# Optimization experiments

Measured on AMD Instinct MI355X. Metric: run time of the kernel, lower is better.

## Reference

```python
import jax, jax.numpy as jnp
import numpy as np

N, F, H, E = 100000, 128, 128, 3200000
EPS = 1e-5


def setup_inputs() -> dict:
    key = jax.random.key(0)
    ks = jax.random.split(key, 16)
    g = lambda k, shape, fan_in: jax.random.normal(k, shape, jnp.float32) / np.sqrt(fan_in)
    inp = {
        'x': jax.random.normal(ks[0], (N, F), jnp.float32),
        'edge_index': jax.random.randint(ks[1], (2, E), 0, N, jnp.int64),
        # SAGEConv params: lin_l (aggregated-neighbor path, has bias), lin_r (root path, no bias)
        'W1l': g(ks[2], (F, H), F), 'b1': jnp.zeros((H,), jnp.float32), 'W1r': g(ks[3], (F, H), F),
        'W2l': g(ks[4], (H, H), H), 'b2': jnp.zeros((H,), jnp.float32), 'W2r': g(ks[5], (H, H), H),
        'W3l': g(ks[6], (H, H), H), 'b3': jnp.zeros((H,), jnp.float32), 'W3r': g(ks[7], (H, H), H),
        'W4l': g(ks[8], (H, 1), H), 'b4': jnp.zeros((1,), jnp.float32), 'W4r': g(ks[9], (H, 1), H),
        # BatchNorm affine params
        'g1': jnp.ones((H,), jnp.float32), 'be1': jnp.zeros((H,), jnp.float32),
        'g2': jnp.ones((H,), jnp.float32), 'be2': jnp.zeros((H,), jnp.float32),
        'g3': jnp.ones((H,), jnp.float32), 'be3': jnp.zeros((H,), jnp.float32),
        # shared residual linear
        'Wlin': g(ks[10], (H, H), H), 'blin': jnp.zeros((H,), jnp.float32),
    }
    return inp


def _sage(x, src, dst, Wl, b, Wr):
    # mean aggregation of source features at destination nodes
    n = x.shape[0]
    s = jax.ops.segment_sum(x[src], dst, num_segments=n)          # [N, d]
    cnt = jax.ops.segment_sum(jnp.ones_like(dst, x.dtype), dst, num_segments=n)
    agg = s / jnp.maximum(cnt, 1.0)[:, None]
    return agg @ Wl + b + x @ Wr


def _bn(x, gamma, beta):
    # training-mode batch norm over node dim (biased variance, as torch)
    mu = x.mean(0)
    var = jnp.mean((x - mu) ** 2, axis=0)
    return gamma * (x - mu) * jax.lax.rsqrt(var + EPS) + beta


def reference(x, edge_index, W1l, b1, W1r, W2l, b2, W2r, W3l, b3, W3r,
              W4l, b4, W4r, g1, be1, g2, be2, g3, be3, Wlin, blin):
    src, dst = edge_index[0], edge_index[1]
    # dropout is identity (eval-mode reference)
    x1 = jax.nn.elu(_bn(_sage(x, src, dst, W1l, b1, W1r), g1, be1))
    x2 = jax.nn.elu(_bn(_sage(x1, src, dst, W2l, b2, W2r), g2, be2))
    x2 = x2 + x1 @ Wlin + blin
    x3 = jax.nn.elu(_bn(_sage(x2, src, dst, W3l, b3, W3r), g3, be3))
    x3 = x3 + x2 @ Wlin + blin
    x4 = _sage(x3, src, dst, W4l, b4, W4r)  # [N, 1]
    return jnp.squeeze(x4, -1)
```

## Files before the change

kernel.cpp:

```cpp
#include <hip/hip_runtime.h>
#include <hip/hip_bf16.h>
#include <math.h>

#define BN_EPS 1e-5f
#define BSTRIDE 96

typedef __attribute__((ext_vector_type(8))) short bf16x8;
typedef __attribute__((ext_vector_type(4))) float f32x4;
typedef unsigned int uint32;

__device__ __forceinline__ unsigned bf16rne(float f) {
  unsigned u = __float_as_uint(f);
  unsigned r = u + 0x7fffu + ((u >> 16) & 1u);
  return r >> 16;
}
__device__ __forceinline__ float bf2f_lo(uint32 u) { return __uint_as_float(u << 16); }
__device__ __forceinline__ float bf2f_hi(uint32 u) { return __uint_as_float(u & 0xffff0000u); }
__device__ __forceinline__ uint32 packbf2(float a, float b) {
  return bf16rne(a) | (bf16rne(b) << 16);
}

__device__ __forceinline__ int edge_at(const int* __restrict__ ei, long long idx, int is64) {
  return is64 ? ei[2 * idx] : ei[idx];
}

__global__ void init_kernel(const int* __restrict__ ei, long long E, int* __restrict__ flag,
                            int* __restrict__ cnt, float* __restrict__ bnsum, int N) {
  if (blockIdx.x == 0) {
    __shared__ int found;
    int t = threadIdx.x;
    if (t == 0) found = 0;
    __syncthreads();
    long long npairs = E < 1024 ? E : 1024;
    for (long long p = t; p < npairs; p += blockDim.x)
      if (ei[2 * p + 1] != 0) found = 1;
    __syncthreads();
    if (t == 0) *flag = found ? 0 : 1;
    return;
  }
  long long i = (blockIdx.x - 1) * (long long)blockDim.x + threadIdx.x;
  if (i < N) cnt[i] = 0;
  else if (i < (long long)N + 64 * 256) bnsum[i - N] = 0.f;
}

__launch_bounds__(256)
__global__ void build_kernel(const int* __restrict__ ei, long long E,
                             const int* __restrict__ flag,
                             int* __restrict__ cnt, int* __restrict__ bkt,
                             const float* __restrict__ x, uint32* __restrict__ xb,
                             long long nf4,
                             const float* __restrict__ Wa, const float* __restrict__ Wb,
                             const float* __restrict__ Wc, const float* __restrict__ Wd,
                             const float* __restrict__ We, const float* __restrict__ Wf,
                             const float* __restrict__ Wg, ushort* __restrict__ Wp,
                             long long K3) {
  long long b = blockIdx.x;
  if (b >= K3) {
    int rb = (int)(b - K3);
    int wi = rb >> 3;
    const float* W = wi == 0 ? Wa : wi == 1 ? Wb : wi == 2 ? Wc : wi == 3 ? Wd
                   : wi == 4 ? We : wi == 5 ? Wf : Wg;
    ushort* dst = Wp + (size_t)wi * 16384;
    int s = (rb & 7) * 256 + threadIdx.x;
    int nt = s >> 8, rem = s & 255, ks = rem >> 6, lane = rem & 63;
    int q = lane >> 4, l16 = lane & 15;
    int kbase = ks * 32 + q * 8, c = nt * 16 + l16;
    uint32 o[4];
#pragma unroll
    for (int jp = 0; jp < 4; ++jp) {
      float fa = W[(size_t)(kbase + 2 * jp) * 128 + c];
      float fb = W[(size_t)(kbase + 2 * jp + 1) * 128 + c];
      o[jp] = packbf2(fa, fb);
    }
    ((uint4*)dst)[s] = make_uint4(o[0], o[1], o[2], o[3]);
    return;
  }
  int role = (int)(b % 3);
  long long id = b / 3;
  if (role == 0) {
    long long g = id * 256 + threadIdx.x;
    long long e0 = 2 * g;
    if (e0 >= E) return;
    int is64 = *flag;
    bool h1 = (e0 + 1 < E);
    int s0, s1 = 0, d0, d1 = 0;
    if (is64 && !(E & 1)) {
      int4 sv = ((const int4*)ei)[g];
      int4 dv = ((const int4*)(ei + 2 * E))[g];
      s0 = sv.x; s1 = sv.z;
      d0 = dv.x; d1 = dv.z;
    } else {
      s0 = edge_at(ei, e0, is64);
      d0 = edge_at(ei, E + e0, is64);
      if (h1) {
        s1 = edge_at(ei, e0 + 1, is64);
        d1 = edge_at(ei, E + e0 + 1, is64);
      }
    }
    int r0 = atomicAdd(&cnt[d0], 1);
    if (r0 < BSTRIDE) bkt[(size_t)d0 * BSTRIDE + r0] = s0;
    if (h1) {
      int r1 = atomicAdd(&cnt[d1], 1);
      if (r1 < BSTRIDE) bkt[(size_t)d1 * BSTRIDE + r1] = s1;
    }
  } else {
    long long i = (id * 2 + (role - 1)) * 256 + threadIdx.x;
    if (i < nf4) {
      float4 f = ((const float4*)x)[i];
      uint2 o2;
      o2.x = packbf2(f.x, f.y);
      o2.y = packbf2(f.z, f.w);
      ((uint2*)xb)[i] = o2;
    }
  }
}

__global__ void aggregate_bf16_kernel(const uint32* __restrict__ X, const int* __restrict__ cnt,
                                      const int* __restrict__ bkt, uint32* __restrict__ out,
                                      int N) {
  int gw = (int)((blockIdx.x * (long long)blockDim.x + threadIdx.x) >> 6);
  int lane = threadIdx.x & 63;
  if (gw >= N) return;
  int deg = cnt[gw];
  if (deg > BSTRIDE) deg = BSTRIDE;
  int b = gw * BSTRIDE, e = b + deg;
  int sub = lane & 15, grp = lane >> 4;
  const uint4* X4 = (const uint4*)X;
  float acc[8];
#pragma unroll
  for (int j = 0; j < 8; ++j) acc[j] = 0.f;
  for (int i = b; i < e; i += 32) {
    uint4 v[8];
#pragma unroll
    for (int u = 0; u < 8; ++u) {
      int ii = i + u * 4 + grp;
      v[u] = make_uint4(0, 0, 0, 0);
      if (ii < e) { int s = bkt[ii]; v[u] = X4[(size_t)s * 16 + sub]; }
    }
#pragma unroll
    for (int u = 0; u < 8; ++u) {
      acc[0] += bf2f_lo(v[u].x); acc[1] += bf2f_hi(v[u].x);
      acc[2] += bf2f_lo(v[u].y); acc[3] += bf2f_hi(v[u].y);
      acc[4] += bf2f_lo(v[u].z); acc[5] += bf2f_hi(v[u].z);
      acc[6] += bf2f_lo(v[u].w); acc[7] += bf2f_hi(v[u].w);
    }
  }
#pragma unroll
  for (int j = 0; j < 8; ++j) {
    acc[j] += __shfl_xor(acc[j], 16, 64);
    acc[j] += __shfl_xor(acc[j], 32, 64);
  }
  if (grp == 0) {
    float inv = 1.0f / fmaxf((float)deg, 1.0f);
    uint4 o;
    o.x = packbf2(acc[0] * inv, acc[1] * inv);
    o.y = packbf2(acc[2] * inv, acc[3] * inv);
    o.z = packbf2(acc[4] * inv, acc[5] * inv);
    o.w = packbf2(acc[6] * inv, acc[7] * inv);
    ((uint4*)out)[(size_t)gw * 16 + sub] = o;
  }
}

__launch_bounds__(256)
__global__ void gemm_mfma_kernel(const ushort* __restrict__ A1, const ushort* __restrict__ W1p,
                                 const ushort* __restrict__ A2, const ushort* __restrict__ W2p,
                                 const ushort* __restrict__ W3p,
                                 const float* __restrict__ bias, const float* __restrict__ rbias,
                                 ushort* __restrict__ Y, ushort* __restrict__ R,
                                 float* __restrict__ bnsum, int N) {
  __shared__ float sred[16][128];
  int t = threadIdx.x;
  int w = t >> 6, lane = t & 63;
  int quad = lane >> 4, l16 = lane & 15;
  int row0 = blockIdx.x * 64 + w * 16;

  f32x4 accY[8], accR[8];
#pragma unroll
  for (int nt = 0; nt < 8; ++nt) {
    accY[nt][0] = accY[nt][1] = accY[nt][2] = accY[nt][3] = 0.f;
    accR[nt][0] = accR[nt][1] = accR[nt][2] = accR[nt][3] = 0.f;
  }

  int rowA = row0 + l16;
  if (rowA > N - 1) rowA = N - 1;
  const ushort* a1p = A1 + (size_t)rowA * 128 + quad * 8;
  const ushort* a2p = A2 + (size_t)rowA * 128 + quad * 8;
  const int haveR = (W3p != nullptr);

#pragma unroll
  for (int ks = 0; ks < 4; ++ks) {
    bf16x8 a = *(const bf16x8*)(a1p + ks * 32);
#pragma unroll
    for (int nt = 0; nt < 8; ++nt) {
      bf16x8 b = *(const bf16x8*)(W1p + ((size_t)(nt * 4 + ks) * 64 + lane) * 8);
      accY[nt] = __builtin_amdgcn_mfma_f32_16x16x32_bf16(a, b, accY[nt], 0, 0, 0);
    }
  }
#pragma unroll
  for (int ks = 0; ks < 4; ++ks) {
    bf16x8 a = *(const bf16x8*)(a2p + ks * 32);
#pragma unroll
    for (int nt = 0; nt < 8; ++nt) {
      bf16x8 b = *(const bf16x8*)(W2p + ((size_t)(nt * 4 + ks) * 64 + lane) * 8);
      accY[nt] = __builtin_amdgcn_mfma_f32_16x16x32_bf16(a, b, accY[nt], 0, 0, 0);
    }
    if (haveR) {
#pragma unroll
      for (int nt = 0; nt < 8; ++nt) {
        bf16x8 b = *(const bf16x8*)(W3p + ((size_t)(nt * 4 + ks) * 64 + lane) * 8);
        accR[nt] = __builtin_amdgcn_mfma_f32_16x16x32_bf16(a, b, accR[nt], 0, 0, 0);
      }
    }
  }

  float s1v[8], s2v[8];
#pragma unroll
  for (int nt = 0; nt < 8; ++nt) {
    int c = nt * 16 + l16;
    float bv = bias[c];
    s1v[nt] = 0.f; s2v[nt] = 0.f;
#pragma unroll
    for (int reg = 0; reg < 4; ++reg) {
      int grow = row0 + quad * 4 + reg;
      if (grow < N) {
        float v = accY[nt][reg] + bv;
        Y[(size_t)grow * 128 + c] = (ushort)bf16rne(v);
        s1v[nt] += v; s2v[nt] += v * v;
      }
    }
    if (haveR) {
      float rb = rbias[c];
#pragma unroll
      for (int reg = 0; reg < 4; ++reg) {
        int grow = row0 + quad * 4 + reg;
        if (grow < N) {
          float v = accR[nt][reg] + rb;
          R[(size_t)grow * 128 + c] = (ushort)bf16rne(v);
        }
      }
    }
  }

  int rrow = w * 4 + quad;
#pragma unroll
  for (int nt = 0; nt < 8; ++nt) sred[rrow][nt * 16 + l16] = s1v[nt];
  __syncthreads();
  if (t < 128) {
    float tot = 0.f;
#pragma unroll
    for (int r16 = 0; r16 < 16; ++r16) tot += sred[r16][t];
    atomicAdd(&bnsum[(size_t)(blockIdx.x & 63) * 256 + t], tot);
  }
  __syncthreads();
#pragma unroll
  for (int nt = 0; nt < 8; ++nt) sred[rrow][nt * 16 + l16] = s2v[nt];
  __syncthreads();
  if (t < 128) {
    float tot = 0.f;
#pragma unroll
    for (int r16 = 0; r16 < 16; ++r16) tot += sred[r16][t];
    atomicAdd(&bnsum[(size_t)(blockIdx.x & 63) * 256 + 128 + t], tot);
  }
}

__global__ void bn_finalize_kernel(float* __restrict__ bnsum, float* __restrict__ bnp, int N) {
  __shared__ float part[256];
  int t = threadIdx.x;
  float a0 = 0.f, a1 = 0.f, a2 = 0.f, a3 = 0.f;
#pragma unroll
  for (int sh = 0; sh < 64; sh += 4) {
    a0 += bnsum[(size_t)(sh + 0) * 256 + t];
    a1 += bnsum[(size_t)(sh + 1) * 256 + t];
    a2 += bnsum[(size_t)(sh + 2) * 256 + t];
    a3 += bnsum[(size_t)(sh + 3) * 256 + t];
  }
  part[t] = (a0 + a1) + (a2 + a3);
  __syncthreads();
  if (t < 128) {
    float invN = 1.0f / (float)N;
    float mu = part[t] * invN;
    float var = part[128 + t] * invN - mu * mu;
    bnp[t] = mu;
    bnp[128 + t] = rsqrtf(var + BN_EPS);
  }
  __syncthreads();
  for (int i = t; i < 64 * 256; i += 256) bnsum[i] = 0.f;
}

__global__ void bn_elu_kernel(const uint4* __restrict__ Y4, const float* __restrict__ bnp,
                              const float* __restrict__ g, const float* __restrict__ be,
                              const uint4* __restrict__ res4, uint4* __restrict__ Xo4,
                              const float* __restrict__ W4l, const float* __restrict__ W4r,
                              float* __restrict__ z, float* __restrict__ rr,
                              long long total4) {
  long long i = blockIdx.x * (long long)blockDim.x + threadIdx.x;
  if (i >= total4) return;
  int c0 = (int)(i & 15) * 8;
  uint4 y = Y4[i];
  float v[8];
  {
    uint32 ww[4] = {y.x, y.y, y.z, y.w};
#pragma unroll
    for (int j = 0; j < 4; ++j) {
      int c = c0 + 2 * j;
      float e0 = g[c]     * (bf2f_lo(ww[j]) - bnp[c])     * bnp[128 + c]     + be[c];
      float e1 = g[c + 1] * (bf2f_hi(ww[j]) - bnp[c + 1]) * bnp[128 + c + 1] + be[c + 1];
      v[2 * j]     = e0 > 0.f ? e0 : expm1f(e0);
      v[2 * j + 1] = e1 > 0.f ? e1 : expm1f(e1);
    }
  }
  if (res4) {
    uint4 rv = res4[i];
    uint32 ww[4] = {rv.x, rv.y, rv.z, rv.w};
#pragma unroll
    for (int j = 0; j < 4; ++j) {
      v[2 * j]     += bf2f_lo(ww[j]);
      v[2 * j + 1] += bf2f_hi(ww[j]);
    }
  }
  if (Xo4) {
    uint4 o;
    o.x = packbf2(v[0], v[1]);
    o.y = packbf2(v[2], v[3]);
    o.z = packbf2(v[4], v[5]);
    o.w = packbf2(v[6], v[7]);
    Xo4[i] = o;
  }
  if (z) {
    float a = 0.f, bb = 0.f;
#pragma unroll
    for (int j = 0; j < 8; ++j) {
      a  += v[j] * W4l[c0 + j];
      bb += v[j] * W4r[c0 + j];
    }
    a  += __shfl_xor(a, 1, 64);  bb += __shfl_xor(bb, 1, 64);
    a  += __shfl_xor(a, 2, 64);  bb += __shfl_xor(bb, 2, 64);
    a  += __shfl_xor(a, 4, 64);  bb += __shfl_xor(bb, 4, 64);
    a  += __shfl_xor(a, 8, 64);  bb += __shfl_xor(bb, 8, 64);
    if ((i & 15) == 0) {
      long long row = i >> 4;
      z[row] = a;
      rr[row] = bb;
    }
  }
}

__global__ void final_kernel(const float* __restrict__ z, const float* __restrict__ rr,
                             const int* __restrict__ cnt, const int* __restrict__ bkt,
                             const float* __restrict__ b4, float* __restrict__ out, int N) {
  long long t = blockIdx.x * (long long)blockDim.x + threadIdx.x;
  int n = (int)(t >> 2);
  int q = (int)(t & 3);
  if (n >= N) n = N - 1;
  int deg = cnt[n];
  if (deg > BSTRIDE) deg = BSTRIDE;
  int b = n * BSTRIDE, e = b + deg;
  float s = 0.f;
  for (int i = b + q; i < e; i += 4) s += z[bkt[i]];
  s += __shfl_xor(s, 1, 64);
  s += __shfl_xor(s, 2, 64);
  if (q == 0) out[n] = s / fmaxf((float)deg, 1.0f) + b4[0] + rr[n];
}

extern "C" void kernel_launch(void* const* d_in, const int* in_sizes, int n_in,
                              void* d_out, int out_size, void* d_ws, size_t ws_size,
                              hipStream_t stream) {
  const float* x   = (const float*)d_in[0];
  const int*   ei  = (const int*)d_in[1];
  const float* W1l = (const float*)d_in[2];
  const float* b1  = (const float*)d_in[3];
  const float* W1r = (const float*)d_in[4];
  const float* W2l = (const float*)d_in[5];
  const float* b2  = (const float*)d_in[6];
  const float* W2r = (const float*)d_in[7];
  const float* W3l = (const float*)d_in[8];
  const float* b3  = (const float*)d_in[9];
  const float* W3r = (const float*)d_in[10];
  const float* W4l = (const float*)d_in[11];
  const float* b4  = (const float*)d_in[12];
  const float* W4r = (const float*)d_in[13];
  const float* g1  = (const float*)d_in[14];
  const float* be1 = (const float*)d_in[15];
  const float* g2  = (const float*)d_in[16];
  const float* be2 = (const float*)d_in[17];
  const float* g3  = (const float*)d_in[18];
  const float* be3 = (const float*)d_in[19];
  const float* Wlin= (const float*)d_in[20];
  const float* blin= (const float*)d_in[21];

  const int N = in_sizes[0] / 128;
  const long long E = in_sizes[1] / 2;
  float* out = (float*)d_out;

  const int B = 256;
  const int gb = (N + 63) / 64;

  char* w = (char*)d_ws;
  size_t o = 0;
  auto alloc = [&](size_t bytes) -> char* {
    char* p = w + o;
    o = (o + bytes + 255) & ~(size_t)255;
    return p;
  };
  int*      cnt   = (int*)alloc((size_t)N * 4);
  int*      flag  = (int*)alloc(4);
  float*    bnsum = (float*)alloc((size_t)64 * 256 * 4);
  float*    bnp   = (float*)alloc(256 * 4);
  float*    z     = (float*)alloc((size_t)N * 4);
  float*    rr    = (float*)alloc((size_t)N * 4);
  ushort*   Wp    = (ushort*)alloc((size_t)7 * 2048 * 16);
  int*      bkt   = (int*)alloc((size_t)N * BSTRIDE * 4);
  char* B1c = alloc((size_t)N * 256);
  char* B2c = alloc((size_t)N * 256);
  char* B3c = alloc((size_t)N * 256);
  (void)ws_size; (void)n_in; (void)out_size;

  uint32* B1 = (uint32*)B1c;
  uint32* B2 = (uint32*)B2c;
  uint32* B3 = (uint32*)B3c;

  const long long pairs = (E + 1) / 2;
  const int ebp = (int)((pairs + B - 1) / B);
  const long long nf4 = (long long)N * 32;
  const int cb4 = (int)((nf4 + B - 1) / B);
  int K = ebp > (cb4 + 1) / 2 ? ebp : (cb4 + 1) / 2;
  const int Gbuild = 3 * K + 56;
  const int zb = 1 + (int)(((long long)N + 64 * 256 + B - 1) / B);
  const int wb = (int)(((long long)N * 64 + B - 1) / B);
  const long long tot4 = (long long)N * 16;
  const int cb = (int)((tot4 + B - 1) / B);
  const int fb = (int)(((long long)N * 4 + B - 1) / B);

  ushort* Wp1l = Wp + 0 * 16384;
  ushort* Wp1r = Wp + 1 * 16384;
  ushort* Wp2l = Wp + 2 * 16384;
  ushort* Wp2r = Wp + 3 * 16384;
  ushort* Wp3l = Wp + 4 * 16384;
  ushort* Wp3r = Wp + 5 * 16384;
  ushort* Wpln = Wp + 6 * 16384;

  init_kernel<<<zb, B, 0, stream>>>(ei, E, flag, cnt, bnsum, N);
  build_kernel<<<Gbuild, B, 0, stream>>>(ei, E, flag, cnt, bkt, x, B2, nf4,
                                         W1l, W1r, W2l, W2r, W3l, W3r, Wlin, Wp,
                                         (long long)3 * K);

  aggregate_bf16_kernel<<<wb, B, 0, stream>>>(B2, cnt, bkt, B1, N);
  gemm_mfma_kernel<<<gb, B, 0, stream>>>((const ushort*)B1, Wp1l, (const ushort*)B2, Wp1r,
                                         nullptr, b1, nullptr, (ushort*)B1, nullptr,
                                         bnsum, N);
  bn_finalize_kernel<<<1, 256, 0, stream>>>(bnsum, bnp, N);
  bn_elu_kernel<<<cb, B, 0, stream>>>((const uint4*)B1, bnp, g1, be1, nullptr, (uint4*)B3,
                                      nullptr, nullptr, nullptr, nullptr, tot4);

  aggregate_bf16_kernel<<<wb, B, 0, stream>>>(B3, cnt, bkt, B1, N);
  gemm_mfma_kernel<<<gb, B, 0, stream>>>((const ushort*)B1, Wp2l, (const ushort*)B3, Wp2r,
                                         Wpln, b2, blin, (ushort*)B1, (ushort*)B2,
                                         bnsum, N);
  bn_finalize_kernel<<<1, 256, 0, stream>>>(bnsum, bnp, N);
  bn_elu_kernel<<<cb, B, 0, stream>>>((const uint4*)B1, bnp, g2, be2, (const uint4*)B2,
                                      (uint4*)B2, nullptr, nullptr, nullptr, nullptr, tot4);

  aggregate_bf16_kernel<<<wb, B, 0, stream>>>(B2, cnt, bkt, B1, N);
  gemm_mfma_kernel<<<gb, B, 0, stream>>>((const ushort*)B1, Wp3l, (const ushort*)B2, Wp3r,
                                         Wpln, b3, blin, (ushort*)B1, (ushort*)B3,
                                         bnsum, N);
  bn_finalize_kernel<<<1, 256, 0, stream>>>(bnsum, bnp, N);
  bn_elu_kernel<<<cb, B, 0, stream>>>((const uint4*)B1, bnp, g3, be3, (const uint4*)B3,
                                      nullptr, W4l, W4r, z, rr, tot4);

  final_kernel<<<fb, B, 0, stream>>>(z, rr, cnt, bkt, b4, out, N);
}
```

Measured before the change: 890.3 us.

## Template GEMM on residual path, use memsets for init, widen final gather

```diff
diff --git a/kernel.cpp b/kernel.cpp
--- a/kernel.cpp
+++ b/kernel.cpp
@@ -24,23 +24,16 @@
   return is64 ? ei[2 * idx] : ei[idx];
 }
 
-__global__ void init_kernel(const int* __restrict__ ei, long long E, int* __restrict__ flag,
-                            int* __restrict__ cnt, float* __restrict__ bnsum, int N) {
-  if (blockIdx.x == 0) {
-    __shared__ int found;
-    int t = threadIdx.x;
-    if (t == 0) found = 0;
-    __syncthreads();
-    long long npairs = E < 1024 ? E : 1024;
-    for (long long p = t; p < npairs; p += blockDim.x)
-      if (ei[2 * p + 1] != 0) found = 1;
-    __syncthreads();
-    if (t == 0) *flag = found ? 0 : 1;
-    return;
-  }
-  long long i = (blockIdx.x - 1) * (long long)blockDim.x + threadIdx.x;
-  if (i < N) cnt[i] = 0;
-  else if (i < (long long)N + 64 * 256) bnsum[i - N] = 0.f;
+__global__ void detect_kernel(const int* __restrict__ ei, long long E, int* __restrict__ flag) {
+  __shared__ int found;
+  int t = threadIdx.x;
+  if (t == 0) found = 0;
+  __syncthreads();
+  long long npairs = E < 1024 ? E : 1024;
+  for (long long p = t; p < npairs; p += blockDim.x)
+    if (ei[2 * p + 1] != 0) found = 1;
+  __syncthreads();
+  if (t == 0) *flag = found ? 0 : 1;
 }
 
 __launch_bounds__(256)
@@ -161,6 +154,7 @@
   }
 }
 
+template <int HR>
 __launch_bounds__(256)
 __global__ void gemm_mfma_kernel(const ushort* __restrict__ A1, const ushort* __restrict__ W1p,
                                  const ushort* __restrict__ A2, const ushort* __restrict__ W2p,
@@ -174,18 +168,19 @@
   int quad = lane >> 4, l16 = lane & 15;
   int row0 = blockIdx.x * 64 + w * 16;
 
-  f32x4 accY[8], accR[8];
+  f32x4 accY[8], accR[HR ? 8 : 1];
 #pragma unroll
   for (int nt = 0; nt < 8; ++nt) {
     accY[nt][0] = accY[nt][1] = accY[nt][2] = accY[nt][3] = 0.f;
-    accR[nt][0] = accR[nt][1] = accR[nt][2] = accR[nt][3] = 0.f;
+    if (HR) {
+      accR[nt][0] = accR[nt][1] = accR[nt][2] = accR[nt][3] = 0.f;
+    }
   }
 
   int rowA = row0 + l16;
   if (rowA > N - 1) rowA = N - 1;
   const ushort* a1p = A1 + (size_t)rowA * 128 + quad * 8;
   const ushort* a2p = A2 + (size_t)rowA * 128 + quad * 8;
-  const int haveR = (W3p != nullptr);
 
 #pragma unroll
   for (int ks = 0; ks < 4; ++ks) {
@@ -204,7 +199,7 @@
       bf16x8 b = *(const bf16x8*)(W2p + ((size_t)(nt * 4 + ks) * 64 + lane) * 8);
       accY[nt] = __builtin_amdgcn_mfma_f32_16x16x32_bf16(a, b, accY[nt], 0, 0, 0);
     }
-    if (haveR) {
+    if (HR) {
 #pragma unroll
       for (int nt = 0; nt < 8; ++nt) {
         bf16x8 b = *(const bf16x8*)(W3p + ((size_t)(nt * 4 + ks) * 64 + lane) * 8);
@@ -218,6 +213,7 @@
   for (int nt = 0; nt < 8; ++nt) {
     int c = nt * 16 + l16;
     float bv = bias[c];
+    float rb = HR ? rbias[c] : 0.f;
     s1v[nt] = 0.f; s2v[nt] = 0.f;
 #pragma unroll
     for (int reg = 0; reg < 4; ++reg) {
@@ -226,16 +222,9 @@
         float v = accY[nt][reg] + bv;
         Y[(size_t)grow * 128 + c] = (ushort)bf16rne(v);
         s1v[nt] += v; s2v[nt] += v * v;
-      }
-    }
-    if (haveR) {
-      float rb = rbias[c];
-#pragma unroll
-      for (int reg = 0; reg < 4; ++reg) {
-        int grow = row0 + quad * 4 + reg;
-        if (grow < N) {
-          float v = accR[nt][reg] + rb;
-          R[(size_t)grow * 128 + c] = (ushort)bf16rne(v);
+        if (HR) {
+          float vr = accR[nt][reg] + rb;
+          R[(size_t)grow * 128 + c] = (ushort)bf16rne(vr);
         }
       }
     }
@@ -349,16 +338,17 @@
                              const int* __restrict__ cnt, const int* __restrict__ bkt,
                              const float* __restrict__ b4, float* __restrict__ out, int N) {
   long long t = blockIdx.x * (long long)blockDim.x + threadIdx.x;
-  int n = (int)(t >> 2);
-  int q = (int)(t & 3);
+  int n = (int)(t >> 3);
+  int q = (int)(t & 7);
   if (n >= N) n = N - 1;
   int deg = cnt[n];
   if (deg > BSTRIDE) deg = BSTRIDE;
   int b = n * BSTRIDE, e = b + deg;
   float s = 0.f;
-  for (int i = b + q; i < e; i += 4) s += z[bkt[i]];
+  for (int i = b + q; i < e; i += 8) s += z[bkt[i]];
   s += __shfl_xor(s, 1, 64);
   s += __shfl_xor(s, 2, 64);
+  s += __shfl_xor(s, 4, 64);
   if (q == 0) out[n] = s / fmaxf((float)deg, 1.0f) + b4[0] + rr[n];
 }
 
@@ -425,11 +415,10 @@
   const int cb4 = (int)((nf4 + B - 1) / B);
   int K = ebp > (cb4 + 1) / 2 ? ebp : (cb4 + 1) / 2;
   const int Gbuild = 3 * K + 56;
-  const int zb = 1 + (int)(((long long)N + 64 * 256 + B - 1) / B);
   const int wb = (int)(((long long)N * 64 + B - 1) / B);
   const long long tot4 = (long long)N * 16;
   const int cb = (int)((tot4 + B - 1) / B);
-  const int fb = (int)(((long long)N * 4 + B - 1) / B);
+  const int fb = (int)(((long long)N * 8 + B - 1) / B);
 
   ushort* Wp1l = Wp + 0 * 16384;
   ushort* Wp1r = Wp + 1 * 16384;
@@ -439,31 +428,33 @@
   ushort* Wp3r = Wp + 5 * 16384;
   ushort* Wpln = Wp + 6 * 16384;
 
-  init_kernel<<<zb, B, 0, stream>>>(ei, E, flag, cnt, bnsum, N);
+  hipMemsetAsync(cnt, 0, (size_t)N * 4, stream);
+  hipMemsetAsync(bnsum, 0, (size_t)64 * 256 * 4, stream);
+  detect_kernel<<<1, 1024, 0, stream>>>(ei, E, flag);
   build_kernel<<<Gbuild, B, 0, stream>>>(ei, E, flag, cnt, bkt, x, B2, nf4,
                                          W1l, W1r, W2l, W2r, W3l, W3r, Wlin, Wp,
                                          (long long)3 * K);
 
   aggregate_bf16_kernel<<<wb, B, 0, stream>>>(B2, cnt, bkt, B1, N);
-  gemm_mfma_kernel<<<gb, B, 0, stream>>>((const ushort*)B1, Wp1l, (const ushort*)B2, Wp1r,
-                                         nullptr, b1, nullptr, (ushort*)B1, nullptr,
-                                         bnsum, N);
+  gemm_mfma_kernel<0><<<gb, B, 0, stream>>>((const ushort*)B1, Wp1l, (const ushort*)B2, Wp1r,
+                                            nullptr, b1, nullptr, (ushort*)B1, nullptr,
+                                            bnsum, N);
   bn_finalize_kernel<<<1, 256, 0, stream>>>(bnsum, bnp, N);
   bn_elu_kernel<<<cb, B, 0, stream>>>((const uint4*)B1, bnp, g1, be1, nullptr, (uint4*)B3,
                                       nullptr, nullptr, nullptr, nullptr, tot4);
 
   aggregate_bf16_kernel<<<wb, B, 0, stream>>>(B3, cnt, bkt, B1, N);
-  gemm_mfma_kernel<<<gb, B, 0, stream>>>((const ushort*)B1, Wp2l, (const ushort*)B3, Wp2r,
-                                         Wpln, b2, blin, (ushort*)B1, (ushort*)B2,
-                                         bnsum, N);
+  gemm_mfma_kernel<1><<<gb, B, 0, stream>>>((const ushort*)B1, Wp2l, (const ushort*)B3, Wp2r,
+                                            Wpln, b2, blin, (ushort*)B1, (ushort*)B2,
+                                            bnsum, N);
   bn_finalize_kernel<<<1, 256, 0, stream>>>(bnsum, bnp, N);
   bn_elu_kernel<<<cb, B, 0, stream>>>((const uint4*)B1, bnp, g2, be2, (const uint4*)B2,
                                       (uint4*)B2, nullptr, nullptr, nullptr, nullptr, tot4);
 
   aggregate_bf16_kernel<<<wb, B, 0, stream>>>(B2, cnt, bkt, B1, N);
-  gemm_mfma_kernel<<<gb, B, 0, stream>>>((const ushort*)B1, Wp3l, (const ushort*)B2, Wp3r,
-                                         Wpln, b3, blin, (ushort*)B1, (ushort*)B3,
-                                         bnsum, N);
+  gemm_mfma_kernel<1><<<gb, B, 0, stream>>>((const ushort*)B1, Wp3l, (const ushort*)B2, Wp3r,
+                                            Wpln, b3, blin, (ushort*)B1, (ushort*)B3,
+                                            bnsum, N);
   bn_finalize_kernel<<<1, 256, 0, stream>>>(bnsum, bnp, N);
   bn_elu_kernel<<<cb, B, 0, stream>>>((const uint4*)B1, bnp, g3, be3, (const uint4*)B3,
                                       nullptr, W4l, W4r, z, rr, tot4);
```

After: 846.7 us. 4.9% less time.
